# Kernel tuning notes

Hardware: AMD Instinct MI355X
Metric: run time of the kernel (lower is better)

## Reference

```python
import jax, jax.numpy as jnp
import numpy as np

NC, NPER, DIN, D, R = 100000, 50000, 128, 128, 7
E = 2100000
ER = E // R  # edges per relation (block layout: relation i owns rows [i*ER, (i+1)*ER))
NEG_SLOPE = 0.2


def _seg_softmax(x, seg, n):
    # numerically-stable softmax over destination-node segments (PyG `softmax`)
    m = jax.ops.segment_max(x, seg, num_segments=n)
    m = jnp.where(jnp.isfinite(m), m, 0.0)  # empty segments -> -inf; neutralize
    e = jnp.exp(x - m[seg])
    s = jax.ops.segment_sum(e, seg, num_segments=n)
    return e / (s[seg] + 1e-16)


def setup_inputs() -> dict:
    key = jax.random.key(0)
    ks = jax.random.split(key, 12)
    N = NC + NPER
    s_in = 1.0 / float(np.sqrt(DIN))
    s_d = 1.0 / float(np.sqrt(D))
    company_emb = jax.random.normal(ks[0], (NC, DIN), jnp.float32)
    person_emb = jax.random.normal(ks[1], (NPER, DIN), jnp.float32)
    edge_index = jax.random.randint(ks[2], (E, 2), 0, N)
    edge_type = jnp.repeat(jnp.arange(R), ER)  # contiguous blocks per relation
    # weights are all-ones except relation 3 -> selects the weighted message branch there
    edge_weight = jnp.ones((E, 1), jnp.float32)
    edge_weight = edge_weight.at[3 * ER:4 * ER].set(
        jax.random.uniform(ks[3], (ER, 1), jnp.float32) + 0.1)
    W_com = jax.random.normal(ks[4], (DIN, D), jnp.float32) * s_in
    W_per = jax.random.normal(ks[5], (DIN, D), jnp.float32) * s_in
    Wq = jax.random.normal(ks[6], (R, D, D), jnp.float32) * s_d
    bq = jnp.zeros((R, D), jnp.float32)
    Wk = jax.random.normal(ks[7], (R, D, D), jnp.float32) * s_d
    bk = jnp.zeros((R, D), jnp.float32)
    Wv = jax.random.normal(ks[8], (D, D), jnp.float32) * s_d
    bv = jnp.zeros((D,), jnp.float32)
    pri = jnp.ones((R,), jnp.float32)
    W_rel_pair = jax.random.normal(ks[9], (R, 2 * D, D), jnp.float32) * s_d  # slot 3 unused
    W_rel3 = jax.random.normal(ks[10], (D, D), jnp.float32) * s_d
    skip = jnp.ones((1,), jnp.float32)
    return {"company_emb": company_emb, "person_emb": person_emb, "edge_weight": edge_weight,
            "W_com": W_com, "W_per": W_per, "Wq": Wq, "bq": bq, "Wk": Wk, "bk": bk,
            "Wv": Wv, "bv": bv, "pri": pri, "W_rel_pair": W_rel_pair, "W_rel3": W_rel3,
            "skip": skip, "edge_index": edge_index, "edge_type": edge_type}


def _hetegnn(company_emb, person_emb, edge_weight, W_com, W_per, Wq, bq, Wk, bk,
             Wv, bv, pri, W_rel_pair, W_rel3, skip, edge_index, edge_type):
    emb = jnp.concatenate([company_emb @ W_com, person_emb @ W_per], axis=0)  # [N, D]
    N = emb.shape[0]
    rs_list = []
    for i in range(R):
        sl = slice(i * ER, (i + 1) * ER)
        src = edge_index[sl, 0]
        dst = edge_index[sl, 1]
        x_j = emb[src]                                   # gathered source features [ER, D]
        if i == 3:  # weighted branch: linear on x_j, scalar scatter-softmax of edge weights
            msg = (x_j @ W_rel3) * _seg_softmax(edge_weight[sl], dst, N)
        else:       # attention branch: rel_wi(concat(x_i, x_j)) -> per-dim scatter-softmax
            temp = jnp.concatenate([emb[dst], x_j], axis=1) @ W_rel_pair[i]  # [ER, D]
            msg = x_j * _seg_softmax(temp, dst, N)
        rs = jax.ops.segment_sum(msg, dst, num_segments=N)  # scatter-add aggregation
        rs_list.append(jax.nn.leaky_relu(rs, NEG_SLOPE))
    rs_stack = jnp.stack(rs_list)                           # [R, N, D]
    # cross-relation attention
    q = jnp.einsum('nd,rde->rne', emb, Wq) + bq[:, None, :]
    k = jnp.einsum('rnd,rde->rne', rs_stack, Wk) + bk[:, None, :]
    scores = (q * k).sum(-1) * pri[:, None] / jnp.sqrt(jnp.float32(D))  # [R, N]
    att = jax.nn.softmax(scores, axis=0)                    # softmax across relations
    v = rs_stack @ Wv + bv                                  # [R, N, D]
    res = jnp.einsum('rn,rnd->nd', att, v)
    res = res + jax.nn.sigmoid(skip) * jax.nn.gelu(emb, approximate=False)
    return res


def reference(company_emb, person_emb, edge_weight, W_com, W_per, Wq, bq, Wk, bk,
              Wv, bv, pri, W_rel_pair, W_rel3, skip, edge_index, edge_type):
    res = _hetegnn(company_emb, person_emb, edge_weight, W_com, W_per, Wq, bq, Wk, bk,
                   Wv, bv, pri, W_rel_pair, W_rel3, skip, edge_index, edge_type)
    return res[:NC], res[NC:]
```

## Files before the change

### kernel.cpp

```cpp
#include <hip/hip_runtime.h>
#include <stdint.h>

#define NCY 100000
#define NPR 50000
#define NT  150000
#define RREL 7
#define ETOT 2100000
#define EREL 300000
#define NSEG (RREL*NT)
#define NEG 0.2f

#define NBUK 256
#define BWID 587
#define P1B  1024
#define CH1  2051
#define EPT  9
#define LSEG (RREL*BWID)
#define SPT  17

#define LSTR 136

typedef __attribute__((ext_vector_type(8))) short short8;
typedef __attribute__((ext_vector_type(4))) float f32x4;
typedef unsigned short u16;

__device__ __forceinline__ float bf2f(u16 h){
  union{unsigned int u; float f;} v; v.u = ((unsigned int)h)<<16; return v.f;
}
__device__ __forceinline__ u16 f2bf(float f){
  union{unsigned int u; float f;} v; v.f=f;
  unsigned int u=v.u;
  return (u16)((u + 0x7fffu + ((u>>16)&1u))>>16);
}
__device__ __forceinline__ float lrelu(float x){ return x>0.f? x : NEG*x; }

#define MFMA(a,b,c) __builtin_amdgcn_mfma_f32_16x16x32_bf16(a,b,c,0,0,0)

__global__ __launch_bounds__(256) void k_bin(const int* __restrict__ eidx,
    const float* __restrict__ ew,
    int* __restrict__ bsrc, int* __restrict__ bkey, float* __restrict__ bew,
    int* __restrict__ gcntT, int* __restrict__ poffT){
  __shared__ int cnt[NBUK];
  __shared__ int pb[NBUK];
  int blk = blockIdx.x, tid = threadIdx.x;
  int base = blk*CH1;
  int n = min(CH1, ETOT-base);
  cnt[tid]=0;
  __syncthreads();
  int esrc[EPT], ekey[EPT], erank[EPT], ebuk[EPT]; float eew[EPT];
  #pragma unroll
  for(int k=0;k<EPT;k++){
    int i = k*256 + tid;
    erank[k]=-1; esrc[k]=0; ekey[k]=0; ebuk[k]=0; eew[k]=0.f;
    if(i<n){
      int e = base+i;
      int2 sd = *(const int2*)(eidx+2*e);
      int r = e/EREL;
      int b = sd.y / BWID;
      esrc[k]=sd.x; ekey[k]=r*NT+sd.y; ebuk[k]=b; eew[k]=ew[e];
      erank[k]=atomicAdd(&cnt[b],1);
    }
  }
  __syncthreads();
  int v = cnt[tid];
  pb[tid]=v; __syncthreads();
  for(int off=1; off<256; off<<=1){
    int a=(tid>=off)?pb[tid-off]:0; __syncthreads();
    pb[tid]+=a; __syncthreads();
  }
  int excl = pb[tid]-v;
  gcntT[blk*NBUK+tid]=v;
  poffT[blk*NBUK+tid]=excl;
  pb[tid]=excl; __syncthreads();
  #pragma unroll
  for(int k=0;k<EPT;k++){
    if(erank[k]>=0){
      int pos = base + pb[ebuk[k]] + erank[k];
      bsrc[pos]=esrc[k]; bkey[pos]=ekey[k]; bew[pos]=eew[k];
    }
  }
}

__global__ __launch_bounds__(256) void k_bsum(const int* __restrict__ gcntT,
                                              int* __restrict__ btot){
  __shared__ int lds[256];
  int b = blockIdx.x, t = threadIdx.x;
  int s=0;
  for(int blk=t; blk<P1B; blk+=256) s += gcntT[blk*NBUK+b];
  lds[t]=s; __syncthreads();
  for(int off=128; off>0; off>>=1){ if(t<off) lds[t]+=lds[t+off]; __syncthreads(); }
  if(t==0) btot[b]=lds[0];
}

__global__ __launch_bounds__(256) void k_bscan(const int* __restrict__ btot,
                                               int* __restrict__ bbase){
  __shared__ int lds[256];
  int t=threadIdx.x;
  int v=btot[t]; lds[t]=v; __syncthreads();
  for(int off=1; off<256; off<<=1){
    int a=(t>=off)?lds[t-off]:0; __syncthreads();
    lds[t]+=a; __syncthreads();
  }
  bbase[t]=lds[t]-v;
}

__global__ __launch_bounds__(256) void k_place(
    const int* __restrict__ bsrc, const int* __restrict__ bkey, const float* __restrict__ bew,
    const int* __restrict__ gcntT, const int* __restrict__ poffT, const int* __restrict__ bbase,
    int* __restrict__ starts_g, int* __restrict__ ends_g,
    int* __restrict__ ssrc, float* __restrict__ sew){
  __shared__ int scnt[LSEG];
  __shared__ int lrun[LSEG];
  __shared__ int gofs[P1B];
  __shared__ int gl[P1B];
  __shared__ int scan[256];
  int b = blockIdx.x, t = threadIdx.x;
  int lo = b*BWID;
  int gbase = bbase[b];
  for(int i=t;i<LSEG;i+=256) scnt[i]=0;
  for(int blk=t; blk<P1B; blk+=256){
    gl[blk]   = gcntT[blk*NBUK+b];
    gofs[blk] = poffT[blk*NBUK+b];
  }
  __syncthreads();
  for(int blk=t; blk<P1B; blk+=256){
    int o = blk*CH1 + gofs[blk], g = gl[blk];
    for(int i=0;i<g;i++){
      int key = bkey[o+i];
      int r = key/NT; int dst = key - r*NT;
      atomicAdd(&scnt[r*BWID + (dst-lo)], 1);
    }
  }
  __syncthreads();
  int ts=0;
  #pragma unroll
  for(int k=0;k<SPT;k++){ int idx=t*SPT+k; ts += (idx<LSEG)? scnt[idx]:0; }
  scan[t]=ts; __syncthreads();
  for(int off=1; off<256; off<<=1){
    int a=(t>=off)?scan[t-off]:0; __syncthreads();
    scan[t]+=a; __syncthreads();
  }
  int run = scan[t]-ts;
  #pragma unroll
  for(int k=0;k<SPT;k++){
    int idx=t*SPT+k;
    if(idx<LSEG){ lrun[idx]=run; run += scnt[idx]; }
  }
  __syncthreads();
  for(int idx=t; idx<LSEG; idx+=256){
    int r = idx/BWID; int ld = idx - r*BWID; int dst = lo+ld;
    if(dst<NT){
      int sgp = gbase + lrun[idx];
      starts_g[r*NT+dst] = sgp;
      ends_g[r*NT+dst]   = sgp + scnt[idx];
    }
  }
  __syncthreads();
  for(int idx=t; idx<LSEG; idx+=256) lrun[idx] += gbase;
  __syncthreads();
  for(int blk=t; blk<P1B; blk+=256){
    int o = blk*CH1 + gofs[blk], g = gl[blk];
    for(int i=0;i<g;i++){
      int key = bkey[o+i];
      int r = key/NT; int dst = key - r*NT;
      int pos = atomicAdd(&lrun[r*BWID+(dst-lo)], 1);
      ssrc[pos] = bsrc[o+i];
      if(r==3) sew[pos] = bew[o+i];
    }
  }
}

__global__ __launch_bounds__(256) void k_prep(const float* __restrict__ Wq, const float* __restrict__ bq,
    const float* __restrict__ Wk, const float* __restrict__ bk,
    float* __restrict__ Ar, float* __restrict__ ur, float* __restrict__ wr,
    float* __restrict__ cr, int* __restrict__ bflag){
  int t = blockIdx.x*256 + threadIdx.x;
  if(t >= RREL*128*128) return;
  int r = t/(128*128); int ij = t - r*128*128; int i = ij>>7, j = ij&127;
  const float* wq = Wq + r*16384; const float* wk = Wk + r*16384;
  float s=0.f;
  for(int k=0;k<128;k++) s += wq[i*128+k]*wk[j*128+k];
  Ar[t] = s;
  if(i==0){
    float su=0.f, sw=0.f;
    for(int k=0;k<128;k++){ su += wq[j*128+k]*bk[r*128+k];
                            sw += wk[j*128+k]*bq[r*128+k]; }
    ur[r*128+j]=su; wr[r*128+j]=sw;
    if(j==0){
      float sc=0.f; int nz=0;
      for(int k=0;k<128;k++){ float a=bq[r*128+k], b2=bk[r*128+k];
        sc += a*b2; nz |= (a!=0.f)||(b2!=0.f); }
      cr[r]=sc; if(nz) atomicOr(bflag,1);
    }
  }
}

struct PackJob{ const float* src; u16* dst; int ksteps; };
struct PackJobs{ PackJob j[20]; };
__global__ __launch_bounds__(256) void k_pack(PackJobs jobs){
  PackJob J = jobs.j[blockIdx.y];
  int t = blockIdx.x*256 + threadIdx.x;
  int lane = t&63, ks=(t>>6)&7, nt=t>>9;
  if(ks >= J.ksteps) return;
  int col = nt*16 + (lane&15);
  int krow = ks*32 + (lane>>4)*8;
  u16* d = J.dst + ((nt*J.ksteps + ks)*64 + lane)*8;
  for(int j=0;j<8;j++) d[j] = f2bf(J.src[(krow+j)*128 + col]);
}

struct GArgs {
  const void* A; const u16* B; int M; int rowoff;
  u16* outH; float* acc; float* den;
  const u16* emb16;
  const float* bv; const float* skip;
};

template<int EPI, int ASRC>
__global__ __launch_bounds__(256) void k_gemm(GArgs G)
{
  int wave = threadIdx.x>>6, lane = threadIdx.x&63;
  int M = G.M;
  int base = blockIdx.x*64 + wave*16;
  if(base >= M) return;
  int arow = base + (lane&15); if(arow >= M) arow = M-1;
  int kof = (lane>>4)*8;
  short8 a[4];
  if(ASRC==0){
    const u16* A = (const u16*)G.A;
    #pragma unroll
    for(int ks=0;ks<4;ks++) a[ks] = *(const short8*)(A + (size_t)arow*128 + ks*32 + kof);
  } else if(ASRC==3){
    const u16* A = (const u16*)G.A;
    float sc = 1.f/G.den[arow];
    #pragma unroll
    for(int ks=0;ks<4;ks++){
      short8 v = *(const short8*)(A + (size_t)arow*128 + ks*32 + kof);
      short8 s;
      #pragma unroll
      for(int j2=0;j2<8;j2++) s[j2]=f2bf(bf2f((u16)v[j2])*sc);
      a[ks]=s;
    }
  } else {
    const float* A = (const float*)G.A;
    #pragma unroll
    for(int ks=0;ks<4;ks++){
      const float* ap = A + (size_t)arow*128 + ks*32 + kof;
      f32x4 lo = *(const f32x4*)ap;
      f32x4 hi = *(const f32x4*)(ap+4);
      short8 s;
      #pragma unroll
      for(int j2=0;j2<4;j2++){ s[j2]=f2bf(lo[j2]); s[4+j2]=f2bf(hi[j2]); }
      a[ks]=s;
    }
  }
  f32x4 acc[8];
  #pragma unroll
  for(int nt=0;nt<8;nt++){
    f32x4 c = {0.f,0.f,0.f,0.f};
    #pragma unroll
    for(int ks=0;ks<4;ks++){
      short8 b = *(const short8*)(G.B + ((nt*4+ks)*64 + lane)*8);
      c = MFMA(a[ks], b, c);
    }
    acc[nt]=c;
  }
  int rbase = base + (lane>>4)*4;
  int cl = lane&15;
  if(EPI==0){
    #pragma unroll
    for(int nt=0;nt<8;nt++)
      for(int j=0;j<4;j++){
        int row=rbase+j;
        if(row<M){
          int col=nt*16+cl;
          G.outH[(size_t)(G.rowoff+row)*128+col] = f2bf(acc[nt][j]);
        }
      }
  } else if(EPI==4){
    #pragma unroll
    for(int nt=0;nt<8;nt++)
      for(int j=0;j<4;j++){
        int row=rbase+j;
        if(row<M){
          int col=nt*16+cl;
          G.outH[(size_t)row*128+col]=f2bf(__expf(acc[nt][j]));
        }
      }
  } else {
    float sg = 1.f/(1.f+__expf(-G.skip[0]));
    #pragma unroll
    for(int nt=0;nt<8;nt++)
      for(int j=0;j<4;j++){
        int row=rbase+j;
        if(row<M){
          int col=nt*16+cl;
          float x = bf2f(G.emb16[(size_t)row*128+col]);
          float g = 0.5f*x*(1.f+erff(x*0.70710678118f));
          G.acc[(size_t)row*128+col] = acc[nt][j] + G.bv[col] + sg*g;
        }
      }
  }
}

struct PArgs {
  const u16* emb16; const int* ssrc; const int* starts_g; const int* ends_g;
  const float* sew;
  const u16* ebR1; const u16* ebR2;
  const u16* pA1; const u16* pA2;
  const u16* pWr3;
  const u16* pB2a; const u16* pB2b; u16* ebW1; u16* ebW2;
  u16* acc16; float* den;
  const float* u1; const float* w1; const float* c1; const float* p1;
  const float* u2; const float* w2; const float* c2; const float* p2;
  const int* bflag;
  int r1, r2;
};

__device__ __forceinline__ void gatherAtt(u16* buf, const u16* __restrict__ ebt,
    const u16* __restrict__ emb16, const int* __restrict__ ssrc,
    const int* __restrict__ sg, const int* __restrict__ eg,
    int rel, int base64, int tid){
  #pragma unroll
  for(int p2=0;p2<2;p2++){
    int ln = (tid>>3) + p2*32;
    int gn = base64 + ln;
    int cb = (tid&7)*16;
    float num[16]={0,0,0,0,0,0,0,0,0,0,0,0,0,0,0,0};
    float den[16]={0,0,0,0,0,0,0,0,0,0,0,0,0,0,0,0};
    if(gn<NT){
      int s=sg[rel*NT+gn], e=eg[rel*NT+gn];
      for(int pos=s;pos<e;pos++){
        int src=ssrc[pos];
        const u16* eb=ebt+(size_t)src*128+cb;
        const u16* xm=emb16+(size_t)src*128+cb;
        short8 e0=*(const short8*)eb, e1=*(const short8*)(eb+8);
        short8 x0=*(const short8*)xm, x1=*(const short8*)(xm+8);
        #pragma unroll
        for(int j=0;j<8;j++){
          float ev0=bf2f((u16)e0[j]), ev1=bf2f((u16)e1[j]);
          num[j]   += bf2f((u16)x0[j])*ev0; den[j]   += ev0;
          num[8+j] += bf2f((u16)x1[j])*ev1; den[8+j] += ev1;
        }
      }
    }
    #pragma unroll
    for(int j=0;j<16;j++) buf[ln*LSTR+cb+j] = f2bf(lrelu(num[j]/(den[j]+1e-16f)));
  }
}

__device__ __forceinline__ void gatherR3(u16* buf, const float* __restrict__ sew,
    const u16* __restrict__ emb16, const int* __restrict__ ssrc,
    const int* __restrict__ sg, const int* __restrict__ eg,
    int base64, int tid){
  #pragma unroll
  for(int p2=0;p2<2;p2++){
    int ln = (tid>>3) + p2*32;
    int gn = base64 + ln;
    int cb = (tid&7)*16;
    float num[16]={0,0,0,0,0,0,0,0,0,0,0,0,0,0,0,0};
    float dn=0.f;
    if(gn<NT){
      int s=sg[3*NT+gn], e=eg[3*NT+gn];
      for(int pos=s;pos<e;pos++){
        int src=ssrc[pos];
        float wv=__expf(sew[pos]);
        dn += wv;
        const u16* xm=emb16+(size_t)src*128+cb;
        short8 x0=*(const short8*)xm, x1=*(const short8*)(xm+8);
        #pragma unroll
        for(int j=0;j<8;j++){
          num[j]   += wv*bf2f((u16)x0[j]);
          num[8+j] += wv*bf2f((u16)x1[j]);
        }
      }
    }
    float inv=1.f/(dn+1e-16f);
    #pragma unroll
    for(int j=0;j<16;j++) buf[ln*LSTR+cb+j] = f2bf(num[j]*inv);
  }
}

template<int NR, int NEB>
__global__ __launch_bounds__(256) void k_fp(PArgs P)
{
  __shared__ u16 lds1[64*LSTR];
  __shared__ u16 lds2[64*LSTR];
  int tid = threadIdx.x;
  int base64 = blockIdx.x*64;
  gatherAtt(lds1, P.ebR1, P.emb16, P.ssrc, P.starts_g, P.ends_g, P.r1, base64, tid);
  if(NR==2) gatherAtt(lds2, P.ebR2, P.emb16, P.ssrc, P.starts_g, P.ends_g, P.r2, base64, tid);
  __syncthreads();
  int wave=tid>>6, lane=tid&63;
  int base = base64 + wave*16;
  if(base >= NT) return;
  int arow = base + (lane&15); if(arow >= NT) arow = NT-1;
  int kof = (lane>>4)*8;
  short8 a[4];
  #pragma unroll
  for(int ks=0;ks<4;ks++) a[ks] = *(const short8*)(P.emb16 + (size_t)arow*128 + ks*32 + kof);
  int rbase = base + (lane>>4)*4;
  int lrb   = wave*16 + (lane>>4)*4;
  int cl = lane&15;
  int bias = *P.bflag;
  float e1v[4], e2v[4];
  {
    f32x4 accS[8];
    #pragma unroll
    for(int nt=0;nt<8;nt++){
      f32x4 c = {0.f,0.f,0.f,0.f};
      #pragma unroll
      for(int ks=0;ks<4;ks++){
        short8 b = *(const short8*)(P.pA1 + ((nt*4+ks)*64 + lane)*8);
        c = MFMA(a[ks], b, c);
      }
      accS[nt]=c;
    }
    float prival = P.p1[0]*0.08838834764831845f;
    #pragma unroll
    for(int j=0;j<4;j++){
      int row=rbase+j; bool ok=row<NT;
      float p=0.f;
      if(ok){
        #pragma unroll
        for(int nt=0;nt<8;nt++){
          int col=nt*16+cl;
          float rv = bf2f(lds1[(lrb+j)*LSTR+col]);
          p += accS[nt][j]*rv;
          if(bias) p += bf2f(P.emb16[(size_t)row*128+col])*P.u1[col] + rv*P.w1[col];
        }
      }
      p += __shfl_xor(p,1,16); p += __shfl_xor(p,2,16);
      p += __shfl_xor(p,4,16); p += __shfl_xor(p,8,16);
      e1v[j] = __expf((p + P.c1[0])*prival);
    }
  }
  if(NR==2){
    f32x4 accS[8];
    #pragma unroll
    for(int nt=0;nt<8;nt++){
      f32x4 c = {0.f,0.f,0.f,0.f};
      #pragma unroll
      for(int ks=0;ks<4;ks++){
        short8 b = *(const short8*)(P.pA2 + ((nt*4+ks)*64 + lane)*8);
        c = MFMA(a[ks], b, c);
      }
      accS[nt]=c;
    }
    float prival = P.p2[0]*0.08838834764831845f;
    #pragma unroll
    for(int j=0;j<4;j++){
      int row=rbase+j; bool ok=row<NT;
      float p=0.f;
      if(ok){
        #pragma unroll
        for(int nt=0;nt<8;nt++){
          int col=nt*16+cl;
          float rv = bf2f(lds2[(lrb+j)*LSTR+col]);
          p += accS[nt][j]*rv;
          if(bias) p += bf2f(P.emb16[(size_t)row*128+col])*P.u2[col] + rv*P.w2[col];
        }
      }
      p += __shfl_xor(p,1,16); p += __shfl_xor(p,2,16);
      p += __shfl_xor(p,4,16); p += __shfl_xor(p,8,16);
      e2v[j] = __expf((p + P.c2[0])*prival);
    }
  }
  #pragma unroll
  for(int j=0;j<4;j++){
    int row=rbase+j;
    if(row<NT){
      float ee1=e1v[j];
      float ee2=(NR==2)? e2v[j] : 0.f;
      #pragma unroll
      for(int nt=0;nt<8;nt++){
        int col=nt*16+cl;
        size_t o=(size_t)row*128+col;
        float add = ee1*bf2f(lds1[(lrb+j)*LSTR+col]);
        if(NR==2) add += ee2*bf2f(lds2[(lrb+j)*LSTR+col]);
        P.acc16[o] = f2bf(bf2f(P.acc16[o]) + add);
      }
      if(cl==0) P.den[row] += ee1 + ee2;
    }
  }
  if(NEB>=1){
    #pragma unroll
    for(int nt=0;nt<8;nt++){
      f32x4 c = {0.f,0.f,0.f,0.f};
      #pragma unroll
      for(int ks=0;ks<4;ks++){
        short8 b = *(const short8*)(P.pB2a + ((nt*4+ks)*64 + lane)*8);
        c = MFMA(a[ks], b, c);
      }
      #pragma unroll
      for(int j=0;j<4;j++){
        int row=rbase+j;
        if(row<NT) P.ebW1[(size_t)row*128 + nt*16+cl] = f2bf(__expf(c[j]));
      }
    }
  }
  if(NEB>=2){
    #pragma unroll
    for(int nt=0;nt<8;nt++){
      f32x4 c = {0.f,0.f,0.f,0.f};
      #pragma unroll
      for(int ks=0;ks<4;ks++){
        short8 b = *(const short8*)(P.pB2b + ((nt*4+ks)*64 + lane)*8);
        c = MFMA(a[ks], b, c);
      }
      #pragma unroll
      for(int j=0;j<4;j++){
        int row=rbase+j;
        if(row<NT) P.ebW2[(size_t)row*128 + nt*16+cl] = f2bf(__expf(c[j]));
      }
    }
  }
}

__global__ __launch_bounds__(256) void k_fp0(PArgs P)
{
  __shared__ u16 lds1[64*LSTR];
  __shared__ u16 lds2[64*LSTR];
  int tid = threadIdx.x;
  int base64 = blockIdx.x*64;
  gatherR3(lds1, P.sew, P.emb16, P.ssrc, P.starts_g, P.ends_g, base64, tid);
  gatherAtt(lds2, P.ebR2, P.emb16, P.ssrc, P.starts_g, P.ends_g, P.r2, base64, tid);
  __syncthreads();
  int wave=tid>>6, lane=tid&63;
  int base = base64 + wave*16;
  if(base >= NT) return;
  int arow = base + (lane&15); if(arow >= NT) arow = NT-1;
  int kof = (lane>>4)*8;
  int lar = wave*16 + (lane&15);
  short8 a[4];
  #pragma unroll
  for(int ks=0;ks<4;ks++) a[ks] = *(const short8*)(P.emb16 + (size_t)arow*128 + ks*32 + kof);
  f32x4 rs3[8];
  {
    short8 ta[4];
    #pragma unroll
    for(int ks=0;ks<4;ks++) ta[ks] = *(const short8*)(lds1 + lar*LSTR + ks*32 + kof);
    #pragma unroll
    for(int nt=0;nt<8;nt++){
      f32x4 c = {0.f,0.f,0.f,0.f};
      #pragma unroll
      for(int ks=0;ks<4;ks++){
        short8 b = *(const short8*)(P.pWr3 + ((nt*4+ks)*64 + lane)*8);
        c = MFMA(ta[ks], b, c);
      }
      #pragma unroll
      for(int j=0;j<4;j++) c[j] = lrelu(c[j]);
      rs3[nt]=c;
    }
  }
  int rbase = base + (lane>>4)*4;
  int lrb   = wave*16 + (lane>>4)*4;
  int cl = lane&15;
  int bias = *P.bflag;
  float e1v[4], e2v[4];
  {
    f32x4 accS[8];
    #pragma unroll
    for(int nt=0;nt<8;nt++){
      f32x4 c = {0.f,0.f,0.f,0.f};
      #pragma unroll
      for(int ks=0;ks<4;ks++){
        short8 b = *(const short8*)(P.pA1 + ((nt*4+ks)*64 + lane)*8);
        c = MFMA(a[ks], b, c);
      }
      accS[nt]=c;
    }
    float prival = P.p1[0]*0.08838834764831845f;
    #pragma unroll
    for(int j=0;j<4;j++){
      int row=rbase+j; bool ok=row<NT;
      float p=0.f;
      if(ok){
        #pragma unroll
        for(int nt=0;nt<8;nt++){
          int col=nt*16+cl;
          float rv = rs3[nt][j];
          p += accS[nt][j]*rv;
          if(bias) p += bf2f(P.emb16[(size_t)row*128+col])*P.u1[col] + rv*P.w1[col];
        }
      }
      p += __shfl_xor(p,1,16); p += __shfl_xor(p,2,16);
      p += __shfl_xor(p,4,16); p += __shfl_xor(p,8,16);
      e1v[j] = __expf((p + P.c1[0])*prival);
    }
  }
  {
    f32x4 accS[8];
    #pragma unroll
    for(int nt=0;nt<8;nt++){
      f32x4 c = {0.f,0.f,0.f,0.f};
      #pragma unroll
      for(int ks=0;ks<4;ks++){
        short8 b = *(const short8*)(P.pA2 + ((nt*4+ks)*64 + lane)*8);
        c = MFMA(a[ks], b, c);
      }
      accS[nt]=c;
    }
    float prival = P.p2[0]*0.08838834764831845f;
    #pragma unroll
    for(int j=0;j<4;j++){
      int row=rbase+j; bool ok=row<NT;
      float p=0.f;
      if(ok){
        #pragma unroll
        for(int nt=0;nt<8;nt++){
          int col=nt*16+cl;
          float rv = bf2f(lds2[(lrb+j)*LSTR+col]);
          p += accS[nt][j]*rv;
          if(bias) p += bf2f(P.emb16[(size_t)row*128+col])*P.u2[col] + rv*P.w2[col];
        }
      }
      p += __shfl_xor(p,1,16); p += __shfl_xor(p,2,16);
      p += __shfl_xor(p,4,16); p += __shfl_xor(p,8,16);
      e2v[j] = __expf((p + P.c2[0])*prival);
    }
  }
  #pragma unroll
  for(int j=0;j<4;j++){
    int row=rbase+j;
    if(row<NT){
      float ee1=e1v[j], ee2=e2v[j];
      #pragma unroll
      for(int nt=0;nt<8;nt++){
        int col=nt*16+cl;
        size_t o=(size_t)row*128+col;
        float add = ee1*bf2f(f2bf(rs3[nt][j])) + ee2*bf2f(lds2[(lrb+j)*LSTR+col]);
        P.acc16[o] = f2bf(bf2f(P.acc16[o]) + add);
      }
      if(cl==0) P.den[row] += ee1 + ee2;
    }
  }
  #pragma unroll
  for(int nt=0;nt<8;nt++){
    f32x4 c = {0.f,0.f,0.f,0.f};
    #pragma unroll
    for(int ks=0;ks<4;ks++){
      short8 b = *(const short8*)(P.pB2a + ((nt*4+ks)*64 + lane)*8);
      c = MFMA(a[ks], b, c);
    }
    #pragma unroll
    for(int j=0;j<4;j++){
      int row=rbase+j;
      if(row<NT) P.ebW1[(size_t)row*128 + nt*16+cl] = f2bf(__expf(c[j]));
    }
  }
  #pragma unroll
  for(int nt=0;nt<8;nt++){
    f32x4 c = {0.f,0.f,0.f,0.f};
    #pragma unroll
    for(int ks=0;ks<4;ks++){
      short8 b = *(const short8*)(P.pB2b + ((nt*4+ks)*64 + lane)*8);
      c = MFMA(a[ks], b, c);
    }
    #pragma unroll
    for(int j=0;j<4;j++){
      int row=rbase+j;
      if(row<NT) P.ebW2[(size_t)row*128 + nt*16+cl] = f2bf(__expf(c[j]));
    }
  }
}

extern "C" void kernel_launch(void* const* d_in, const int* in_sizes, int n_in,
                              void* d_out, int out_size, void* d_ws, size_t ws_size,
                              hipStream_t stream){
  const float* company = (const float*)d_in[0];
  const float* person  = (const float*)d_in[1];
  const float* eweight = (const float*)d_in[2];
  const float* W_com   = (const float*)d_in[3];
  const float* W_per   = (const float*)d_in[4];
  const float* Wq      = (const float*)d_in[5];
  const float* bq      = (const float*)d_in[6];
  const float* Wk      = (const float*)d_in[7];
  const float* bk      = (const float*)d_in[8];
  const float* Wv      = (const float*)d_in[9];
  const float* bvv     = (const float*)d_in[10];
  const float* pri     = (const float*)d_in[11];
  const float* Wpair   = (const float*)d_in[12];
  const float* Wrel3   = (const float*)d_in[13];
  const float* skip    = (const float*)d_in[14];
  const int*   eidx    = (const int*)d_in[15];
  float* out = (float*)d_out;

  char* w = (char*)d_ws;
  auto alloc = [&](size_t sz)->void*{ void* p=(void*)w; w += (sz+255)&~(size_t)255; return p; };
  u16*   emb16 = (u16*)alloc((size_t)NT*128*2);
  u16*   ebA   = (u16*)alloc((size_t)NT*128*2);
  u16*   ebB   = (u16*)alloc((size_t)NT*128*2);
  u16*   acc16 = (u16*)alloc((size_t)NT*128*2);
  float* den   = (float*)alloc((size_t)NT*4);
  int*   starts_g = (int*)alloc((size_t)NSEG*4);
  int*   ends_g   = (int*)alloc((size_t)NSEG*4);
  int*   ssrc  = (int*)alloc((size_t)ETOT*4);
  float* sew   = (float*)alloc((size_t)ETOT*4);
  float* Ar    = (float*)alloc((size_t)RREL*16384*4);
  float* ur    = (float*)alloc(RREL*128*4);
  float* wr    = (float*)alloc(RREL*128*4);
  float* cr    = (float*)alloc(RREL*4);
  int*   bflag = (int*)alloc(256);
  u16* pWcom  = (u16*)alloc(16384*2);
  u16* pWper  = (u16*)alloc(16384*2);
  u16* pWrel3 = (u16*)alloc(16384*2);
  u16* pWv    = (u16*)alloc(16384*2);
  u16* pAr    = (u16*)alloc((size_t)RREL*16384*2);
  u16* pWbot  = (u16*)alloc((size_t)6*16384*2);
  (void)ws_size; (void)in_sizes; (void)n_in; (void)out_size;

  u16* ebC = (u16*)d_out;
  u16* ebD = ebC + (size_t)NT*128;

  int*   bsrc  = (int*)ebA;
  int*   bkey  = bsrc + ETOT;
  float* bew   = (float*)(bkey + ETOT);
  int*   gcntT = (int*)acc16;
  int*   poffT = gcntT + P1B*NBUK;
  int*   btot  = poffT + P1B*NBUK;
  int*   bbase = btot + NBUK;

  hipMemsetAsync(den, 0, (size_t)NT*4, stream);
  hipMemsetAsync(bflag, 0, 4, stream);

  k_bin<<<P1B,256,0,stream>>>(eidx, eweight, bsrc, bkey, bew, gcntT, poffT);
  k_bsum<<<NBUK,256,0,stream>>>(gcntT, btot);
  k_bscan<<<1,256,0,stream>>>(btot, bbase);
  k_place<<<NBUK,256,0,stream>>>(bsrc,bkey,bew,gcntT,poffT,bbase,
                                 starts_g,ends_g,ssrc,sew);
  hipMemsetAsync(acc16, 0, (size_t)NT*128*2, stream);

  k_prep<<<(RREL*16384+255)/256,256,0,stream>>>(Wq,bq,Wk,bk,Ar,ur,wr,cr,bflag);

  const int attr[6] = {0,1,2,4,5,6};
  PackJobs pj{};
  int nj=0;
  auto addjob=[&](const float* s,u16* d,int ks){ pj.j[nj].src=s; pj.j[nj].dst=d; pj.j[nj].ksteps=ks; nj++; };
  addjob(W_com,pWcom,4); addjob(W_per,pWper,4);
  addjob(Wrel3,pWrel3,4); addjob(Wv,pWv,4);
  for(int r=0;r<RREL;r++) addjob(Ar + (size_t)r*16384, pAr + (size_t)r*16384, 4);
  for(int i=0;i<6;i++) addjob(Wpair + (size_t)attr[i]*32768 + 16384, pWbot + (size_t)i*16384, 4);
  dim3 pg(16, nj);
  k_pack<<<pg,256,0,stream>>>(pj);

  GArgs g{};
  g = GArgs{}; g.A=company; g.B=pWcom; g.M=NCY; g.rowoff=0; g.outH=emb16;
  k_gemm<0,1><<<(NCY+63)/64,256,0,stream>>>(g);
  g = GArgs{}; g.A=person; g.B=pWper; g.M=NPR; g.rowoff=NCY; g.outH=emb16;
  k_gemm<0,1><<<(NPR+63)/64,256,0,stream>>>(g);

  g = GArgs{}; g.A=emb16; g.B=pWbot; g.M=NT; g.outH=ebA;
  k_gemm<4,0><<<(NT+63)/64,256,0,stream>>>(g);

  int NBLK = (NT+63)/64;
  auto mkP = [&](int r1,int r2,const u16* eb1,const u16* eb2,
                 int sa,int sb,u16* w1,u16* w2)->PArgs{
    PArgs P{};
    P.emb16=emb16; P.ssrc=ssrc; P.starts_g=starts_g; P.ends_g=ends_g; P.sew=sew;
    P.ebR1=eb1; P.ebR2=eb2;
    P.pA1=pAr+(size_t)r1*16384; P.pA2=pAr+(size_t)r2*16384;
    P.pWr3=pWrel3;
    P.pB2a=(sa>=0)? pWbot+(size_t)sa*16384 : nullptr;
    P.pB2b=(sb>=0)? pWbot+(size_t)sb*16384 : nullptr;
    P.ebW1=w1; P.ebW2=w2;
    P.acc16=acc16; P.den=den;
    P.u1=ur+(size_t)r1*128; P.w1=wr+(size_t)r1*128; P.c1=cr+r1; P.p1=pri+r1;
    P.u2=ur+(size_t)r2*128; P.w2=wr+(size_t)r2*128; P.c2=cr+r2; P.p2=pri+r2;
    P.bflag=bflag; P.r1=r1; P.r2=r2;
    return P;
  };

  k_fp0<<<NBLK,256,0,stream>>>(mkP(3,0, nullptr,ebA, 1,2, ebC,ebD));
  k_fp<2,2><<<NBLK,256,0,stream>>>(mkP(1,2, ebC,ebD, 3,4, ebA,ebB));
  k_fp<2,1><<<NBLK,256,0,stream>>>(mkP(4,5, ebA,ebB, 5,-1, ebC,nullptr));
  k_fp<1,0><<<NBLK,256,0,stream>>>(mkP(6,6, ebC,nullptr, -1,-1, nullptr,nullptr));

  g = GArgs{}; g.A=acc16; g.B=pWv; g.M=NT;
  g.acc=out; g.den=den; g.emb16=emb16; g.bv=bvv; g.skip=skip;
  k_gemm<3,3><<<(NT+63)/64,256,0,stream>>>(g);
}
```

Measured before the change: 904.9 us.

## Swizzle LDS tiles, unroll gathers by two, raise occupancy hints

Drops the padded LDS row stride in favour of an XOR-swizzled layout, so shared memory per block shrinks while bank conflicts stay low. The gather loops now process two edges per iteration to put more loads in flight, and write results with vectorized 16-byte stores. k_fp sizes its LDS buffer to the number of relations it uses, and both kernels get a launch-bounds occupancy hint of 5 blocks. The extra loads and the occupancy hint could raise register pressure or cause spills.

Result: slower. 964.3 us (+6.6%).

```diff
diff --git a/kernel.cpp b/kernel.cpp
--- a/kernel.cpp
+++ b/kernel.cpp
@@ -18,7 +18,7 @@
 #define LSEG (RREL*BWID)
 #define SPT  17
 
-#define LSTR 136
+#define LSTR 128
 
 typedef __attribute__((ext_vector_type(8))) short short8;
 typedef __attribute__((ext_vector_type(4))) float f32x4;
@@ -33,6 +33,9 @@
   return (u16)((u + 0x7fffu + ((u>>16)&1u))>>16);
 }
 __device__ __forceinline__ float lrelu(float x){ return x>0.f? x : NEG*x; }
+__device__ __forceinline__ int lidx(int row, int col){
+  return row*LSTR + ((((col>>4)^(row&7)))<<4) + (col&15);
+}
 
 #define MFMA(a,b,c) __builtin_amdgcn_mfma_f32_16x16x32_bf16(a,b,c,0,0,0)
 
@@ -329,22 +332,48 @@
     float den[16]={0,0,0,0,0,0,0,0,0,0,0,0,0,0,0,0};
     if(gn<NT){
       int s=sg[rel*NT+gn], e=eg[rel*NT+gn];
-      for(int pos=s;pos<e;pos++){
-        int src=ssrc[pos];
-        const u16* eb=ebt+(size_t)src*128+cb;
-        const u16* xm=emb16+(size_t)src*128+cb;
-        short8 e0=*(const short8*)eb, e1=*(const short8*)(eb+8);
-        short8 x0=*(const short8*)xm, x1=*(const short8*)(xm+8);
+      int pos=s;
+      for(; pos+1<e; pos+=2){
+        int s0=ssrc[pos], s1=ssrc[pos+1];
+        const u16* eb0=ebt+(size_t)s0*128+cb;   const u16* xm0=emb16+(size_t)s0*128+cb;
+        const u16* eb1=ebt+(size_t)s1*128+cb;   const u16* xm1=emb16+(size_t)s1*128+cb;
+        short8 ea0=*(const short8*)eb0, ea1=*(const short8*)(eb0+8);
+        short8 xa0=*(const short8*)xm0, xa1=*(const short8*)(xm0+8);
+        short8 eb0v=*(const short8*)eb1, eb1v=*(const short8*)(eb1+8);
+        short8 xb0=*(const short8*)xm1, xb1=*(const short8*)(xm1+8);
         #pragma unroll
         for(int j=0;j<8;j++){
-          float ev0=bf2f((u16)e0[j]), ev1=bf2f((u16)e1[j]);
-          num[j]   += bf2f((u16)x0[j])*ev0; den[j]   += ev0;
-          num[8+j] += bf2f((u16)x1[j])*ev1; den[8+j] += ev1;
-        }
-      }
-    }
-    #pragma unroll
-    for(int j=0;j<16;j++) buf[ln*LSTR+cb+j] = f2bf(lrelu(num[j]/(den[j]+1e-16f)));
+          float e00=bf2f((u16)ea0[j]), e01=bf2f((u16)ea1[j]);
+          float e10=bf2f((u16)eb0v[j]), e11=bf2f((u16)eb1v[j]);
+          num[j]   += bf2f((u16)xa0[j])*e00 + bf2f((u16)xb0[j])*e10;
+          den[j]   += e00 + e10;
+          num[8+j] += bf2f((u16)xa1[j])*e01 + bf2f((u16)xb1[j])*e11;
+          den[8+j] += e01 + e11;
+        }
+      }
+      if(pos<e){
+        int s0=ssrc[pos];
+        const u16* eb0=ebt+(size_t)s0*128+cb;  const u16* xm0=emb16+(size_t)s0*128+cb;
+        short8 ea0=*(const short8*)eb0, ea1=*(const short8*)(eb0+8);
+        short8 xa0=*(const short8*)xm0, xa1=*(const short8*)(xm0+8);
+        #pragma unroll
+        for(int j=0;j<8;j++){
+          float e00=bf2f((u16)ea0[j]), e01=bf2f((u16)ea1[j]);
+          num[j]   += bf2f((u16)xa0[j])*e00; den[j]   += e00;
+          num[8+j] += bf2f((u16)xa1[j])*e01; den[8+j] += e01;
+        }
+      }
+    }
+    short8 v0, v1;
+    #pragma unroll
+    for(int j=0;j<8;j++){
+      v0[j] = (short)f2bf(lrelu(num[j]/(den[j]+1e-16f)));
+      v1[j] = (short)f2bf(lrelu(num[8+j]/(den[8+j]+1e-16f)));
+    }
+    int g1 = (tid&7) ^ (ln&7);
+    u16* wp = buf + ln*LSTR + g1*16;
+    *(short8*)wp = v0;
+    *(short8*)(wp+8) = v1;
   }
 }
 
@@ -375,16 +404,25 @@
       }
     }
     float inv=1.f/(dn+1e-16f);
-    #pragma unroll
-    for(int j=0;j<16;j++) buf[ln*LSTR+cb+j] = f2bf(num[j]*inv);
+    short8 v0, v1;
+    #pragma unroll
+    for(int j=0;j<8;j++){
+      v0[j] = (short)f2bf(num[j]*inv);
+      v1[j] = (short)f2bf(num[8+j]*inv);
+    }
+    int g1 = (tid&7) ^ (ln&7);
+    u16* wp = buf + ln*LSTR + g1*16;
+    *(short8*)wp = v0;
+    *(short8*)(wp+8) = v1;
   }
 }
 
 template<int NR, int NEB>
-__global__ __launch_bounds__(256) void k_fp(PArgs P)
+__global__ __launch_bounds__(256,5) void k_fp(PArgs P)
 {
-  __shared__ u16 lds1[64*LSTR];
-  __shared__ u16 lds2[64*LSTR];
+  __shared__ u16 ldsA[(NR==2 ? 2 : 1)*64*LSTR];
+  u16* lds1 = ldsA;
+  u16* lds2 = ldsA + (NR==2 ? 64*LSTR : 0);
   int tid = threadIdx.x;
   int base64 = blockIdx.x*64;
   gatherAtt(lds1, P.ebR1, P.emb16, P.ssrc, P.starts_g, P.ends_g, P.r1, base64, tid);
@@ -424,7 +462,7 @@
         #pragma unroll
         for(int nt=0;nt<8;nt++){
           int col=nt*16+cl;
-          float rv = bf2f(lds1[(lrb+j)*LSTR+col]);
+          float rv = bf2f(lds1[lidx(lrb+j,col)]);
           p += accS[nt][j]*rv;
           if(bias) p += bf2f(P.emb16[(size_t)row*128+col])*P.u1[col] + rv*P.w1[col];
         }
@@ -455,7 +493,7 @@
         #pragma unroll
         for(int nt=0;nt<8;nt++){
           int col=nt*16+cl;
-          float rv = bf2f(lds2[(lrb+j)*LSTR+col]);
+          float rv = bf2f(lds2[lidx(lrb+j,col)]);
           p += accS[nt][j]*rv;
           if(bias) p += bf2f(P.emb16[(size_t)row*128+col])*P.u2[col] + rv*P.w2[col];
         }
@@ -475,8 +513,8 @@
       for(int nt=0;nt<8;nt++){
         int col=nt*16+cl;
         size_t o=(size_t)row*128+col;
-        float add = ee1*bf2f(lds1[(lrb+j)*LSTR+col]);
-        if(NR==2) add += ee2*bf2f(lds2[(lrb+j)*LSTR+col]);
+        float add = ee1*bf2f(lds1[lidx(lrb+j,col)]);
+        if(NR==2) add += ee2*bf2f(lds2[lidx(lrb+j,col)]);
         P.acc16[o] = f2bf(bf2f(P.acc16[o]) + add);
       }
       if(cl==0) P.den[row] += ee1 + ee2;
@@ -516,7 +554,7 @@
   }
 }
 
-__global__ __launch_bounds__(256) void k_fp0(PArgs P)
+__global__ __launch_bounds__(256,5) void k_fp0(PArgs P)
 {
   __shared__ u16 lds1[64*LSTR];
   __shared__ u16 lds2[64*LSTR];
@@ -529,7 +567,8 @@
   int base = base64 + wave*16;
   if(base >= NT) return;
   int arow = base + (lane&15); if(arow >= NT) arow = NT-1;
-  int kof = (lane>>4)*8;
+  int hi = lane>>4;
+  int kof = hi*8;
   int lar = wave*16 + (lane&15);
   short8 a[4];
   #pragma unroll
@@ -538,7 +577,10 @@
   {
     short8 ta[4];
     #pragma unroll
-    for(int ks=0;ks<4;ks++) ta[ks] = *(const short8*)(lds1 + lar*LSTR + ks*32 + kof);
+    for(int ks=0;ks<4;ks++){
+      int g = ((ks<<1)+(hi>>1)) ^ (lar&7);
+      ta[ks] = *(const short8*)(lds1 + lar*LSTR + g*16 + ((hi&1)<<3));
+    }
     #pragma unroll
     for(int nt=0;nt<8;nt++){
       f32x4 c = {0.f,0.f,0.f,0.f};
@@ -609,7 +651,7 @@
         #pragma unroll
         for(int nt=0;nt<8;nt++){
           int col=nt*16+cl;
-          float rv = bf2f(lds2[(lrb+j)*LSTR+col]);
+          float rv = bf2f(lds2[lidx(lrb+j,col)]);
           p += accS[nt][j]*rv;
           if(bias) p += bf2f(P.emb16[(size_t)row*128+col])*P.u2[col] + rv*P.w2[col];
         }
@@ -628,7 +670,7 @@
       for(int nt=0;nt<8;nt++){
         int col=nt*16+cl;
         size_t o=(size_t)row*128+col;
-        float add = ee1*bf2f(f2bf(rs3[nt][j])) + ee2*bf2f(lds2[(lrb+j)*LSTR+col]);
+        float add = ee1*bf2f(f2bf(rs3[nt][j])) + ee2*bf2f(lds2[lidx(lrb+j,col)]);
         P.acc16[o] = f2bf(bf2f(P.acc16[o]) + add);
       }
       if(cl==0) P.den[row] += ee1 + ee2;
```
